# Optimization experiments

Measured on AMD Instinct MI355X. Metric: run time of the kernel, lower is better.

Reference implementation:

```python
import jax, jax.numpy as jnp
import numpy as np

CONV_LAYERS = 1
BI_GRU_LAYERS = 2
BN_EPS = 1e-3


def _bn(x, gamma, beta, mean, var):
    return gamma * (x - mean) * jax.lax.rsqrt(var + BN_EPS) + beta


def _gru_pass(x, Wx, Wh, b_in, b_rec, reverse=False):
    # Keras GRU: reset_after=True, recurrent_activation=sigmoid, activation=relu,
    # gate order [z, r, h]. x: [B,T,D] -> [B,T,U]
    B, T, _ = x.shape
    U = Wh.shape[0]
    if reverse:
        x = x[:, ::-1]
    xg = jnp.einsum('btd,dg->btg', x, Wx) + b_in  # [B,T,3U] input-side gates, precomputed
    xg = jnp.swapaxes(xg, 0, 1)                    # time-major [T,B,3U]

    def step(h, g):
        rg = h @ Wh + b_rec                        # recurrent-side gates [B,3U]
        xz, xr, xh = jnp.split(g, 3, axis=-1)
        rz, rr, rh = jnp.split(rg, 3, axis=-1)
        z = jax.nn.sigmoid(xz + rz)
        r = jax.nn.sigmoid(xr + rr)
        hh = jax.nn.relu(xh + r * rh)              # reset_after: r gates the recurrent term
        h = z * h + (1.0 - z) * hh
        return h, h

    h0 = jnp.zeros((B, U), x.dtype)
    _, hs = jax.lax.scan(step, h0, xg)             # [T,B,U]
    hs = jnp.swapaxes(hs, 0, 1)
    if reverse:
        hs = hs[:, ::-1]
    return hs


def setup_inputs() -> dict:
    key = jax.random.key(0)
    ks = jax.random.split(key, 16)
    B, T, F = 32, 1024, 80
    C, U, V, K = 512, 512, 1024, 11
    s = 0.02
    inp = {
        'x': jax.random.normal(ks[0], (B, T, F), jnp.float32),
        'conv_w': jax.random.normal(ks[1], (K, F, C), jnp.float32) * s,
        'conv_b': jnp.zeros((C,), jnp.float32),
        'gru_fwd_wx': jax.random.normal(ks[2], (C, 3 * U), jnp.float32) * s,
        'gru_fwd_wh': jax.random.normal(ks[3], (U, 3 * U), jnp.float32) * s,
        'gru_fwd_bi': jnp.zeros((3 * U,), jnp.float32),
        'gru_fwd_br': jnp.zeros((3 * U,), jnp.float32),
        'gru_bwd_wx': jax.random.normal(ks[4], (C, 3 * U), jnp.float32) * s,
        'gru_bwd_wh': jax.random.normal(ks[5], (U, 3 * U), jnp.float32) * s,
        'gru_bwd_bi': jnp.zeros((3 * U,), jnp.float32),
        'gru_bwd_br': jnp.zeros((3 * U,), jnp.float32),
        'gamma': jnp.ones((C,), jnp.float32) + 0.1 * jax.random.normal(ks[6], (C,), jnp.float32),
        'beta': 0.1 * jax.random.normal(ks[7], (C,), jnp.float32),
        'mov_mean': jnp.zeros((C,), jnp.float32),
        'mov_var': jnp.ones((C,), jnp.float32),
        'dense_w': jax.random.normal(ks[8], (U, V), jnp.float32) * s,
        'dense_b': jnp.zeros((V,), jnp.float32),
    }
    return inp


def reference(x, conv_w, conv_b, gru_fwd_wx, gru_fwd_wh, gru_fwd_bi, gru_fwd_br,
              gru_bwd_wx, gru_bwd_wh, gru_bwd_bi, gru_bwd_br,
              gamma, beta, mov_mean, mov_var, dense_w, dense_b):
    for _ in range(CONV_LAYERS):
        x = jax.lax.conv_general_dilated(
            x, conv_w, window_strides=(2,), padding='SAME',
            dimension_numbers=('NWC', 'WIO', 'NWC'))
        x = jax.nn.relu(x + conv_b)
    x = _bn(x, gamma, beta, mov_mean, mov_var)  # same BN layer reused in source
    for _ in range(BI_GRU_LAYERS):              # same BiGRU layer (shared weights) reused
        x = (_gru_pass(x, gru_fwd_wx, gru_fwd_wh, gru_fwd_bi, gru_fwd_br, reverse=False)
             + _gru_pass(x, gru_bwd_wx, gru_bwd_wh, gru_bwd_bi, gru_bwd_br, reverse=True))
    x = _bn(x, gamma, beta, mov_mean, mov_var)
    logits = jnp.einsum('btu,uv->btv', x, dense_w) + dense_b
    return jax.nn.softmax(logits, axis=-1)
```

## Files before the change

kernel.cpp:

```cpp
#include <hip/hip_runtime.h>
#include <hip/hip_fp16.h>

#define BB 32
#define CC 512
#define UU 512
#define GG 1536
#define VV 1024
#define TT 512
#define MM (BB*TT)
#define TIN 1024
#define FIN 80
#define EPS 1e-3f
#define SENT 0xFFFFFFFFu

typedef _Float16 h8 __attribute__((ext_vector_type(8)));
typedef float f4 __attribute__((ext_vector_type(4)));

__global__ __launch_bounds__(256) void conv_bn_k(
    const float* __restrict__ x, const float* __restrict__ w, const float* __restrict__ cb,
    const float* __restrict__ gam, const float* __restrict__ bet,
    const float* __restrict__ mu_, const float* __restrict__ var_,
    __half* __restrict__ out)
{
  __shared__ float xs[41*80];
  int tg = blockIdx.x, b = blockIdx.y, ch = blockIdx.z;
  int t0 = tg*16;
  int in0 = t0*2 - 4;
  for (int i = threadIdx.x; i < 41*80; i += 256) {
    int r = i / 80, f = i - r*80;
    int ri = in0 + r;
    xs[i] = (ri >= 0 && ri < TIN) ? x[((size_t)b*TIN + ri)*FIN + f] : 0.f;
  }
  __syncthreads();
  int c = ch*256 + threadIdx.x;
  float acc[16];
  float bv = cb[c];
#pragma unroll
  for (int i = 0; i < 16; i++) acc[i] = bv;
  for (int k = 0; k < 11; k++) {
    for (int f = 0; f < 80; f++) {
      float wv = w[((size_t)k*80 + f)*CC + c];
#pragma unroll
      for (int i = 0; i < 16; i++) acc[i] += xs[(2*i + k)*80 + f] * wv;
    }
  }
  float ga = gam[c], be = bet[c], mu = mu_[c], iv = rsqrtf(var_[c] + EPS);
#pragma unroll
  for (int i = 0; i < 16; i++) {
    float v = fmaxf(acc[i], 0.f);
    out[((size_t)b*TT + t0 + i)*CC + c] = __float2half(ga*(v - mu)*iv + be);
  }
}

__global__ __launch_bounds__(256) void prep_wx_k(
    const float* __restrict__ wxf, const float* __restrict__ wxb,
    __half* __restrict__ of, __half* __restrict__ ob)
{
  __shared__ float tile[64][65];
  int kt = blockIdx.x*64, nt = blockIdx.y*64;
  const float* src = blockIdx.z ? wxb : wxf;
  __half* dst = blockIdx.z ? ob : of;
  for (int i = threadIdx.x; i < 4096; i += 256) {
    int r = i >> 6, c = i & 63;
    tile[r][c] = src[(size_t)(kt+r)*GG + nt + c];
  }
  __syncthreads();
  for (int i = threadIdx.x; i < 4096; i += 256) {
    int r = i >> 6, c = i & 63;
    __half h = __float2half(tile[c][r]);
    dst[(size_t)(nt+r)*1024 + kt + c] = h;
    dst[(size_t)(nt+r)*1024 + 512 + kt + c] = h;
  }
}

__global__ __launch_bounds__(256) void prep_dense_k(
    const float* __restrict__ dw, const float* __restrict__ gam, const float* __restrict__ var_,
    __half* __restrict__ dst)
{
  __shared__ float tile[64][65];
  __shared__ float s64[64];
  int kt = blockIdx.x*64, nt = blockIdx.y*64;
  if (threadIdx.x < 64) {
    int k = kt + threadIdx.x;
    s64[threadIdx.x] = gam[k] * rsqrtf(var_[k] + EPS);
  }
  for (int i = threadIdx.x; i < 4096; i += 256) {
    int r = i >> 6, c = i & 63;
    tile[r][c] = dw[(size_t)(kt+r)*VV + nt + c];
  }
  __syncthreads();
  for (int i = threadIdx.x; i < 4096; i += 256) {
    int r = i >> 6, c = i & 63;
    __half h = __float2half(tile[c][r] * s64[c]);
    dst[(size_t)(nt+r)*1024 + kt + c] = h;
    dst[(size_t)(nt+r)*1024 + 512 + kt + c] = h;
  }
}

__global__ __launch_bounds__(256) void prep_bias_k(
    const float* __restrict__ dw, const float* __restrict__ db,
    const float* __restrict__ gam, const float* __restrict__ bet,
    const float* __restrict__ mu_, const float* __restrict__ var_,
    float* __restrict__ bias2)
{
  int n = blockIdx.x*256 + threadIdx.x;
  float acc = db[n];
  for (int k = 0; k < CC; k++) {
    float o = bet[k] - gam[k]*mu_[k]*rsqrtf(var_[k] + EPS);
    acc += o * dw[(size_t)k*VV + n];
  }
  bias2[n] = acc;
}

template<int OUTH>
__global__ __launch_bounds__(256,2) void hgemm_k(
    const __half* __restrict__ A, const __half* __restrict__ BT,
    const float* __restrict__ bias, void* __restrict__ Cout,
    int M, int N, int K, int lda, int ldb)
{
  __shared__ _Float16 As[128*40];
  __shared__ _Float16 Bs[128*40];
  int m0 = blockIdx.y*128, n0 = blockIdx.x*128;
  int tid = threadIdx.x;
  int l = tid & 63, w = tid >> 6;
  int wr = w >> 1, wc = w & 1;
  int srow = tid >> 1, soff = (tid & 1)*16;
  const __half* ap = A  + (size_t)(m0 + srow)*lda + soff;
  const __half* bp = BT + (size_t)(n0 + srow)*ldb + soff;
  f4 acc[4][4];
#pragma unroll
  for (int i=0;i<4;i++)
#pragma unroll
    for (int j=0;j<4;j++) acc[i][j] = (f4){0.f,0.f,0.f,0.f};

  uint4 av  = *(const uint4*)(ap);
  uint4 av2 = *(const uint4*)(ap + 8);
  uint4 bv  = *(const uint4*)(bp);
  uint4 bv2 = *(const uint4*)(bp + 8);
  int lr = (l & 15), lk = (l >> 4)*8;
  for (int k0 = 0; k0 < K; k0 += 32) {
    __syncthreads();
    *(uint4*)&As[srow*40 + soff]     = av;
    *(uint4*)&As[srow*40 + soff + 8] = av2;
    *(uint4*)&Bs[srow*40 + soff]     = bv;
    *(uint4*)&Bs[srow*40 + soff + 8] = bv2;
    __syncthreads();
    if (k0 + 32 < K) {
      av  = *(const uint4*)(ap + k0 + 32);
      av2 = *(const uint4*)(ap + k0 + 40);
      bv  = *(const uint4*)(bp + k0 + 32);
      bv2 = *(const uint4*)(bp + k0 + 40);
    }
    h8 af[4], bf[4];
#pragma unroll
    for (int i = 0; i < 4; i++)
      af[i] = *(const h8*)&As[(wr*64 + i*16 + lr)*40 + lk];
#pragma unroll
    for (int j = 0; j < 4; j++)
      bf[j] = *(const h8*)&Bs[(wc*64 + j*16 + lr)*40 + lk];
#pragma unroll
    for (int i = 0; i < 4; i++)
#pragma unroll
      for (int j = 0; j < 4; j++)
        acc[i][j] = __builtin_amdgcn_mfma_f32_16x16x32_f16(af[i], bf[j], acc[i][j], 0, 0, 0);
  }
  int cb = n0 + wc*64 + lr;
  int rb = m0 + wr*64 + (l >> 4)*4;
#pragma unroll
  for (int j = 0; j < 4; j++) {
    float bs = bias[cb + j*16];
#pragma unroll
    for (int i = 0; i < 4; i++) {
#pragma unroll
      for (int q = 0; q < 4; q++) {
        float v = acc[i][j][q] + bs;
        int row = rb + i*16 + q, col = cb + j*16;
        if (OUTH) ((__half*)Cout)[(size_t)row*N + col] = __float2half(v);
        else      ((float*)Cout)[(size_t)row*N + col] = v;
      }
    }
  }
}

__global__ __launch_bounds__(256,1) void gru_layer_k(
    const __half* __restrict__ xgf, const __half* __restrict__ xgb,
    const float* __restrict__ whf, const float* __restrict__ whb,
    const float* __restrict__ brf, const float* __restrict__ brb,
    __half* __restrict__ H,
    unsigned* __restrict__ hbL)
{
  int wg  = blockIdx.x & 31;
  int bg  = (blockIdx.x >> 5) & 3;
  int dir = blockIdx.x >> 7;
  int grp = dir*4 + bg;
  const __half* xg = dir ? xgb : xgf;
  const float* wh  = dir ? whb : whf;
  const float* brc = dir ? brb : brf;
  unsigned* hbg = hbL + (size_t)grp*8192;
  int tid = threadIdx.x;
  int u0 = wg*16, b0 = bg*8;
  int l = tid & 63, wv = tid >> 6;

  __shared__ _Float16 hsl[16*512];
  __shared__ float S[4*3*64*4];

  h8 wb[3][4];
  {
    int n = l & 15, kb = (l >> 4)*8;
#pragma unroll
    for (int t = 0; t < 3; t++) {
      int col = t*512 + u0 + n;
#pragma unroll
      for (int ks = 0; ks < 4; ks++) {
        int k0 = wv*128 + ks*32 + kb;
        h8 v;
#pragma unroll
        for (int j = 0; j < 8; j++)
          v[j] = (_Float16)wh[(size_t)(k0+j)*GG + col];
        wb[t][ks] = v;
      }
    }
  }
  for (int i = tid; i < 4096; i += 256)
    *(unsigned*)&hsl[8*512 + i*2] = 0u;

  int gb_ = tid >> 3, up = tid & 7;
  float br3[3][2];
  float hreg[2] = {0.f, 0.f};
  unsigned xzr = 0, xrr = 0, xhr = 0;
  if (tid < 64) {
    int u = u0 + up*2;
#pragma unroll
    for (int g = 0; g < 3; g++) { br3[g][0] = brc[g*512+u]; br3[g][1] = brc[g*512+u+1]; }
    __hip_atomic_store(&hbg[(0*32 + wg)*64 + tid], 0u,
                       __ATOMIC_RELAXED, __HIP_MEMORY_SCOPE_AGENT);
    int t0_ = dir ? 511 : 0;
    const unsigned* xp = (const unsigned*)xg + (size_t)((b0+gb_)*TT + t0_)*768;
    xzr = xp[(u0>>1) + up];
    xrr = xp[256 + (u0>>1) + up];
    xhr = xp[512 + (u0>>1) + up];
  }

  int sidx = tid - 64, srw = sidx >> 2, sq = sidx & 3;

#define STAGE_PHASE(PH) {                                                   \
    const unsigned* gp = &hbg[((PH)*32 + srw)*64 + sq*16];                  \
    uint4 d0, d1, d2, d3;                                                   \
    long guard = 0;                                                         \
    for (;;) {                                                              \
      asm volatile(                                                         \
        "global_load_dwordx4 %0, %4, off sc0 sc1\n\t"                       \
        "global_load_dwordx4 %1, %4, off offset:16 sc0 sc1\n\t"             \
        "global_load_dwordx4 %2, %4, off offset:32 sc0 sc1\n\t"             \
        "global_load_dwordx4 %3, %4, off offset:48 sc0 sc1\n\t"             \
        "s_waitcnt vmcnt(0)"                                                \
        : "=&v"(d0),"=&v"(d1),"=&v"(d2),"=&v"(d3) : "v"(gp) : "memory");    \
      bool ok = (d0.x!=SENT)&(d0.y!=SENT)&(d0.z!=SENT)&(d0.w!=SENT)         \
              & (d1.x!=SENT)&(d1.y!=SENT)&(d1.z!=SENT)&(d1.w!=SENT)         \
              & (d2.x!=SENT)&(d2.y!=SENT)&(d2.z!=SENT)&(d2.w!=SENT)         \
              & (d3.x!=SENT)&(d3.y!=SENT)&(d3.z!=SENT)&(d3.w!=SENT);        \
      if (ok || ++guard > 3000000L) break;                                  \
    }                                                                       \
    int r0_ = sq*2, r1_ = sq*2 + 1, g0_ = srw*2;                            \
    *(uint4*)&hsl[r0_*512 + (((g0_  ) ^ r0_) << 3)] = d0;                   \
    *(uint4*)&hsl[r0_*512 + (((g0_+1) ^ r0_) << 3)] = d1;                   \
    *(uint4*)&hsl[r1_*512 + (((g0_  ) ^ r1_) << 3)] = d2;                   \
    *(uint4*)&hsl[r1_*512 + (((g0_+1) ^ r1_) << 3)] = d3;                   \
  }

  if (tid >= 64 && tid < 192) STAGE_PHASE(0);
  __syncthreads();

  for (int s = 0; s < 512; s++) {
    f4 a0 = (f4){0.f,0.f,0.f,0.f}, a1 = a0, a2 = a0;
#pragma unroll
    for (int ks = 0; ks < 4; ks++) {
      int g = wv*16 + ks*4 + (l >> 4);
      h8 af = *(const h8*)&hsl[(l & 15)*512 + ((g ^ (l & 7)) << 3)];
      a0 = __builtin_amdgcn_mfma_f32_16x16x32_f16(af, wb[0][ks], a0, 0, 0, 0);
      a1 = __builtin_amdgcn_mfma_f32_16x16x32_f16(af, wb[1][ks], a1, 0, 0, 0);
      a2 = __builtin_amdgcn_mfma_f32_16x16x32_f16(af, wb[2][ks], a2, 0, 0, 0);
    }
    *(f4*)&S[((wv*3 + 0)*64 + l)*4] = a0;
    *(f4*)&S[((wv*3 + 1)*64 + l)*4] = a1;
    *(f4*)&S[((wv*3 + 2)*64 + l)*4] = a2;
    if (tid < 64)
      __hip_atomic_store(&hbg[(((s+2)&3)*32 + wg)*64 + tid], SENT,
                         __ATOMIC_RELAXED, __HIP_MEMORY_SCOPE_AGENT);
    __syncthreads();
    int pn = (s + 1) & 3;
    if (tid < 64) {
      int lane_ = (gb_ >> 2)*16 + up*2;
      int q = gb_ & 3;
      float rgv[3][2];
#pragma unroll
      for (int g3 = 0; g3 < 3; g3++) {
#pragma unroll
        for (int e = 0; e < 2; e++) {
          float a = br3[g3][e];
#pragma unroll
          for (int w = 0; w < 4; w++)
            a += S[((w*3 + g3)*64 + lane_ + e)*4 + q];
          rgv[g3][e] = a;
        }
      }
      __half2 xzh = *(__half2*)&xzr, xrh = *(__half2*)&xrr, xhh = *(__half2*)&xhr;
      float2 xzv = __half22float2(xzh), xrv = __half22float2(xrh), xhv = __half22float2(xhh);
      float xzf[2] = {xzv.x, xzv.y}, xrf[2] = {xrv.x, xrv.y}, xhf[2] = {xhv.x, xhv.y};
#pragma unroll
      for (int e = 0; e < 2; e++) {
        float z = 1.f/(1.f + __expf(-(xzf[e] + rgv[0][e])));
        float r = 1.f/(1.f + __expf(-(xrf[e] + rgv[1][e])));
        float hh = fmaxf(xhf[e] + r*rgv[2][e], 0.f);
        hreg[e] = z*hreg[e] + (1.f - z)*hh;
      }
      __half2 hp2 = __floats2half2_rn(hreg[0], hreg[1]);
      unsigned pk = *(unsigned*)&hp2;
      __hip_atomic_store(&hbg[(pn*32 + wg)*64 + tid], pk,
                         __ATOMIC_RELAXED, __HIP_MEMORY_SCOPE_AGENT);
      int t = dir ? (511 - s) : s;
      ((unsigned*)H)[(size_t)((b0+gb_)*TT + t)*512 + dir*256 + (u0>>1) + up] = pk;
      int tn = (dir ? (510 - s) : (s + 1)) & 511;
      const unsigned* xp = (const unsigned*)xg + (size_t)((b0+gb_)*TT + tn)*768;
      xzr = xp[(u0>>1) + up];
      xrr = xp[256 + (u0>>1) + up];
      xhr = xp[512 + (u0>>1) + up];
    } else if (tid < 192) {
      STAGE_PHASE(pn);
    }
    __syncthreads();
  }
#undef STAGE_PHASE
}

__global__ __launch_bounds__(256) void softmax_k(float* __restrict__ p) {
  size_t row = blockIdx.x;
  float* pr = p + row*VV;
  int tid = threadIdx.x;
  float4 v = ((float4*)pr)[tid];
  float m = fmaxf(fmaxf(v.x, v.y), fmaxf(v.z, v.w));
#pragma unroll
  for (int o = 32; o >= 1; o >>= 1) m = fmaxf(m, __shfl_xor(m, o));
  __shared__ float red[4];
  __shared__ float red2[4];
  int w = tid >> 6;
  if ((tid & 63) == 0) red[w] = m;
  __syncthreads();
  m = fmaxf(fmaxf(red[0], red[1]), fmaxf(red[2], red[3]));
  v.x = __expf(v.x - m); v.y = __expf(v.y - m);
  v.z = __expf(v.z - m); v.w = __expf(v.w - m);
  float s = v.x + v.y + v.z + v.w;
#pragma unroll
  for (int o = 32; o >= 1; o >>= 1) s += __shfl_xor(s, o);
  if ((tid & 63) == 0) red2[w] = s;
  __syncthreads();
  s = red2[0] + red2[1] + red2[2] + red2[3];
  float inv = 1.f / s;
  v.x *= inv; v.y *= inv; v.z *= inv; v.w *= inv;
  ((float4*)pr)[tid] = v;
}

extern "C" void kernel_launch(void* const* d_in, const int* in_sizes, int n_in,
                              void* d_out, int out_size, void* d_ws, size_t ws_size,
                              hipStream_t stream) {
  const float* x      = (const float*)d_in[0];
  const float* conv_w = (const float*)d_in[1];
  const float* conv_b = (const float*)d_in[2];
  const float* wx_f   = (const float*)d_in[3];
  const float* wh_f   = (const float*)d_in[4];
  const float* bi_f   = (const float*)d_in[5];
  const float* br_f   = (const float*)d_in[6];
  const float* wx_b   = (const float*)d_in[7];
  const float* wh_b   = (const float*)d_in[8];
  const float* bi_b   = (const float*)d_in[9];
  const float* br_b   = (const float*)d_in[10];
  const float* gam    = (const float*)d_in[11];
  const float* bet    = (const float*)d_in[12];
  const float* mu_    = (const float*)d_in[13];
  const float* var_   = (const float*)d_in[14];
  const float* dw     = (const float*)d_in[15];
  const float* db     = (const float*)d_in[16];

  char* ws = (char*)d_ws;
  __half* xgf   = (__half*)(ws + 0);
  __half* xgb   = (__half*)(ws + 50331648LL);
  __half* WxfT2 = (__half*)(ws + 100663296LL);
  __half* WxbT2 = (__half*)(ws + 103809024LL);
  __half* DwT2  = (__half*)(ws + 106954752LL);
  float*  bias2 = (float*)(ws + 109051904LL);
  __half* c0    = (__half*)(ws + 109056000LL);
  __half* H     = (__half*)(ws + 109056000LL);
  unsigned* hb1 = (unsigned*)(ws + 142610432LL);
  unsigned* hb2 = (unsigned*)(ws + 142872576LL);
  if (ws_size < 143134720ULL) return;
  float* logits = (float*)d_out;

  hipMemsetAsync(hb1, 0xFF, 524288, stream);

  prep_wx_k<<<dim3(8,24,2), 256, 0, stream>>>(wx_f, wx_b, WxfT2, WxbT2);
  prep_dense_k<<<dim3(8,16), 256, 0, stream>>>(dw, gam, var_, DwT2);
  prep_bias_k<<<4, 256, 0, stream>>>(dw, db, gam, bet, mu_, var_, bias2);

  conv_bn_k<<<dim3(32,32,2), 256, 0, stream>>>(x, conv_w, conv_b, gam, bet, mu_, var_, c0);

  hgemm_k<1><<<dim3(12,128), 256, 0, stream>>>(c0, WxfT2, bi_f, xgf, MM, GG, 512, 512, 1024);
  hgemm_k<1><<<dim3(12,128), 256, 0, stream>>>(c0, WxbT2, bi_b, xgb, MM, GG, 512, 512, 1024);
  gru_layer_k<<<256, 256, 0, stream>>>(xgf, xgb, wh_f, wh_b, br_f, br_b, H, hb1);
  hgemm_k<1><<<dim3(12,128), 256, 0, stream>>>(H, WxfT2, bi_f, xgf, MM, GG, 1024, 1024, 1024);
  hgemm_k<1><<<dim3(12,128), 256, 0, stream>>>(H, WxbT2, bi_b, xgb, MM, GG, 1024, 1024, 1024);
  gru_layer_k<<<256, 256, 0, stream>>>(xgf, xgb, wh_f, wh_b, br_f, br_b, H, hb2);
  hgemm_k<0><<<dim3(8,128), 256, 0, stream>>>(H, DwT2, bias2, logits, MM, VV, 1024, 1024, 1024);
  softmax_k<<<MM, 256, 0, stream>>>(logits);
}
```

Baseline: 2.890 ms.

## Repartition GRU recurrence to 64 blocks with full-K per wave and double-buffered h

The persistent GRU kernel now runs 64 blocks instead of 256. Each wave owns 16 hidden units over the full K=512 reduction, using swapped MFMA operands with a 3x16 register-resident weight tile. This removes the cross-wave shared-memory reduction and the separate gate-computing threads, so all lanes do gate math and all threads poll the global h exchange. The h staging in LDS is double-buffered, leaving one barrier per step. The cost is far more registers per thread, more MFMA work per block, and fewer CUs working on the latency-bound recurrence.

```diff
diff --git a/kernel.cpp b/kernel.cpp
--- a/kernel.cpp
+++ b/kernel.cpp
@@ -189,148 +189,138 @@
     __half* __restrict__ H,
     unsigned* __restrict__ hbL)
 {
-  int wg  = blockIdx.x & 31;
-  int bg  = (blockIdx.x >> 5) & 3;
-  int dir = blockIdx.x >> 7;
+  int wg  = blockIdx.x & 7;
+  int bg  = (blockIdx.x >> 3) & 3;
+  int dir = blockIdx.x >> 5;
   int grp = dir*4 + bg;
   const __half* xg = dir ? xgb : xgf;
   const float* wh  = dir ? whb : whf;
   const float* brc = dir ? brb : brf;
   unsigned* hbg = hbL + (size_t)grp*8192;
   int tid = threadIdx.x;
-  int u0 = wg*16, b0 = bg*8;
-  int l = tid & 63, wv = tid >> 6;
-
-  __shared__ _Float16 hsl[16*512];
-  __shared__ float S[4*3*64*4];
-
-  h8 wb[3][4];
+  int L = tid & 63, wv = tid >> 6;
+  int u0 = wg*64, b0 = bg*8;
+
+  __shared__ _Float16 hsl[2][8][512];
+
+  int urow = L & 15, kb = L >> 4;
+  int ubase = u0 + wv*16;
+  h8 wb[3][16];
+#pragma unroll
+  for (int g3 = 0; g3 < 3; g3++)
+#pragma unroll
+    for (int ks = 0; ks < 16; ks++) {
+      h8 v;
+#pragma unroll
+      for (int j = 0; j < 8; j++)
+        v[j] = (_Float16)wh[(size_t)(ks*32 + kb*8 + j)*GG + g3*512 + ubase + urow];
+      wb[g3][ks] = v;
+    }
+
+  int b = L & 15, b7 = L & 7;
+  int myu = ubase + kb*4;
+  float br3[3][4];
+#pragma unroll
+  for (int g3 = 0; g3 < 3; g3++)
+#pragma unroll
+    for (int q = 0; q < 4; q++)
+      br3[g3][q] = brc[g3*512 + myu + q];
+  float hreg[4] = {0.f, 0.f, 0.f, 0.f};
+  bool bval = b < 8;
+  int upair = (u0 >> 1) + wv*8 + kb*2;
+
+  uint2 xz2, xr2, xh2;
   {
-    int n = l & 15, kb = (l >> 4)*8;
-#pragma unroll
-    for (int t = 0; t < 3; t++) {
-      int col = t*512 + u0 + n;
-#pragma unroll
-      for (int ks = 0; ks < 4; ks++) {
-        int k0 = wv*128 + ks*32 + kb;
-        h8 v;
-#pragma unroll
-        for (int j = 0; j < 8; j++)
-          v[j] = (_Float16)wh[(size_t)(k0+j)*GG + col];
-        wb[t][ks] = v;
-      }
-    }
-  }
-  for (int i = tid; i < 4096; i += 256)
-    *(unsigned*)&hsl[8*512 + i*2] = 0u;
-
-  int gb_ = tid >> 3, up = tid & 7;
-  float br3[3][2];
-  float hreg[2] = {0.f, 0.f};
-  unsigned xzr = 0, xrr = 0, xhr = 0;
-  if (tid < 64) {
-    int u = u0 + up*2;
-#pragma unroll
-    for (int g = 0; g < 3; g++) { br3[g][0] = brc[g*512+u]; br3[g][1] = brc[g*512+u+1]; }
-    __hip_atomic_store(&hbg[(0*32 + wg)*64 + tid], 0u,
-                       __ATOMIC_RELAXED, __HIP_MEMORY_SCOPE_AGENT);
     int t0_ = dir ? 511 : 0;
-    const unsigned* xp = (const unsigned*)xg + (size_t)((b0+gb_)*TT + t0_)*768;
-    xzr = xp[(u0>>1) + up];
-    xrr = xp[256 + (u0>>1) + up];
-    xhr = xp[512 + (u0>>1) + up];
-  }
-
-  int sidx = tid - 64, srw = sidx >> 2, sq = sidx & 3;
-
-#define STAGE_PHASE(PH) {                                                   \
-    const unsigned* gp = &hbg[((PH)*32 + srw)*64 + sq*16];                  \
-    uint4 d0, d1, d2, d3;                                                   \
+    const unsigned* xp = (const unsigned*)xg + (size_t)((b0 + b7)*TT + t0_)*768;
+    xz2 = *(const uint2*)(xp + upair);
+    xr2 = *(const uint2*)(xp + 256 + upair);
+    xh2 = *(const uint2*)(xp + 512 + upair);
+  }
+
+  __hip_atomic_store(&hbg[0*2048 + wg*256 + tid], 0u,
+                     __ATOMIC_RELAXED, __HIP_MEMORY_SCOPE_AGENT);
+
+  int sr = tid >> 5, sc = tid & 31;
+  int sb = sc >> 2, sg0 = sr*8 + (sc & 3)*2;
+  int sws0 = ((sg0 ^ sb) << 3), sws1 = (((sg0 + 1) ^ sb) << 3);
+
+#define STAGE(PH, NB) {                                                     \
+    const unsigned* gp = &hbg[(PH)*2048 + sr*256 + sc*8];                   \
+    uint4 d0, d1;                                                           \
     long guard = 0;                                                         \
     for (;;) {                                                              \
       asm volatile(                                                         \
-        "global_load_dwordx4 %0, %4, off sc0 sc1\n\t"                       \
-        "global_load_dwordx4 %1, %4, off offset:16 sc0 sc1\n\t"             \
-        "global_load_dwordx4 %2, %4, off offset:32 sc0 sc1\n\t"             \
-        "global_load_dwordx4 %3, %4, off offset:48 sc0 sc1\n\t"             \
+        "global_load_dwordx4 %0, %2, off sc0 sc1\n\t"                       \
+        "global_load_dwordx4 %1, %2, off offset:16 sc0 sc1\n\t"             \
         "s_waitcnt vmcnt(0)"                                                \
-        : "=&v"(d0),"=&v"(d1),"=&v"(d2),"=&v"(d3) : "v"(gp) : "memory");    \
+        : "=&v"(d0), "=&v"(d1) : "v"(gp) : "memory");                       \
       bool ok = (d0.x!=SENT)&(d0.y!=SENT)&(d0.z!=SENT)&(d0.w!=SENT)         \
-              & (d1.x!=SENT)&(d1.y!=SENT)&(d1.z!=SENT)&(d1.w!=SENT)         \
-              & (d2.x!=SENT)&(d2.y!=SENT)&(d2.z!=SENT)&(d2.w!=SENT)         \
-              & (d3.x!=SENT)&(d3.y!=SENT)&(d3.z!=SENT)&(d3.w!=SENT);        \
+              & (d1.x!=SENT)&(d1.y!=SENT)&(d1.z!=SENT)&(d1.w!=SENT);        \
       if (ok || ++guard > 3000000L) break;                                  \
     }                                                                       \
-    int r0_ = sq*2, r1_ = sq*2 + 1, g0_ = srw*2;                            \
-    *(uint4*)&hsl[r0_*512 + (((g0_  ) ^ r0_) << 3)] = d0;                   \
-    *(uint4*)&hsl[r0_*512 + (((g0_+1) ^ r0_) << 3)] = d1;                   \
-    *(uint4*)&hsl[r1_*512 + (((g0_  ) ^ r1_) << 3)] = d2;                   \
-    *(uint4*)&hsl[r1_*512 + (((g0_+1) ^ r1_) << 3)] = d3;                   \
-  }
-
-  if (tid >= 64 && tid < 192) STAGE_PHASE(0);
+    *(uint4*)&hsl[NB][sb][sws0] = d0;                                       \
+    *(uint4*)&hsl[NB][sb][sws1] = d1;                                       \
+  }
+
+  STAGE(0, 0);
   __syncthreads();
 
   for (int s = 0; s < 512; s++) {
+    int buf = s & 1;
+    __hip_atomic_store(&hbg[((s+3)&3)*2048 + wg*256 + tid], SENT,
+                       __ATOMIC_RELAXED, __HIP_MEMORY_SCOPE_AGENT);
     f4 a0 = (f4){0.f,0.f,0.f,0.f}, a1 = a0, a2 = a0;
 #pragma unroll
-    for (int ks = 0; ks < 4; ks++) {
-      int g = wv*16 + ks*4 + (l >> 4);
-      h8 af = *(const h8*)&hsl[(l & 15)*512 + ((g ^ (l & 7)) << 3)];
-      a0 = __builtin_amdgcn_mfma_f32_16x16x32_f16(af, wb[0][ks], a0, 0, 0, 0);
-      a1 = __builtin_amdgcn_mfma_f32_16x16x32_f16(af, wb[1][ks], a1, 0, 0, 0);
-      a2 = __builtin_amdgcn_mfma_f32_16x16x32_f16(af, wb[2][ks], a2, 0, 0, 0);
-    }
-    *(f4*)&S[((wv*3 + 0)*64 + l)*4] = a0;
-    *(f4*)&S[((wv*3 + 1)*64 + l)*4] = a1;
-    *(f4*)&S[((wv*3 + 2)*64 + l)*4] = a2;
-    if (tid < 64)
-      __hip_atomic_store(&hbg[(((s+2)&3)*32 + wg)*64 + tid], SENT,
-                         __ATOMIC_RELAXED, __HIP_MEMORY_SCOPE_AGENT);
+    for (int ks = 0; ks < 16; ks++) {
+      int g = ks*4 + kb;
+      h8 hf = *(const h8*)&hsl[buf][b7][(g ^ b7) << 3];
+      a0 = __builtin_amdgcn_mfma_f32_16x16x32_f16(wb[0][ks], hf, a0, 0, 0, 0);
+      a1 = __builtin_amdgcn_mfma_f32_16x16x32_f16(wb[1][ks], hf, a1, 0, 0, 0);
+      a2 = __builtin_amdgcn_mfma_f32_16x16x32_f16(wb[2][ks], hf, a2, 0, 0, 0);
+    }
+    int t = dir ? (511 - s) : s;
+    __half2 xzl = *(__half2*)&xz2.x, xzh = *(__half2*)&xz2.y;
+    __half2 xrl = *(__half2*)&xr2.x, xrh = *(__half2*)&xr2.y;
+    __half2 xhl = *(__half2*)&xh2.x, xhh = *(__half2*)&xh2.y;
+    float2 fz0 = __half22float2(xzl), fz1 = __half22float2(xzh);
+    float2 fr0 = __half22float2(xrl), fr1 = __half22float2(xrh);
+    float2 fh0 = __half22float2(xhl), fh1 = __half22float2(xhh);
+    float xzf[4] = {fz0.x, fz0.y, fz1.x, fz1.y};
+    float xrf[4] = {fr0.x, fr0.y, fr1.x, fr1.y};
+    float xhf[4] = {fh0.x, fh0.y, fh1.x, fh1.y};
+#pragma unroll
+    for (int q = 0; q < 4; q++) {
+      float az = (q==0? a0[0] : q==1? a0[1] : q==2? a0[2] : a0[3]);
+      float ar = (q==0? a1[0] : q==1? a1[1] : q==2? a1[2] : a1[3]);
+      float ah = (q==0? a2[0] : q==1? a2[1] : q==2? a2[2] : a2[3]);
+      float z = 1.f/(1.f + __expf(-(xzf[q] + br3[0][q] + az)));
+      float r = 1.f/(1.f + __expf(-(xrf[q] + br3[1][q] + ar)));
+      float hh = fmaxf(xhf[q] + r*(br3[2][q] + ah), 0.f);
+      hreg[q] = z*hreg[q] + (1.f - z)*hh;
+    }
+    int pn = (s + 1) & 3;
+    if (bval) {
+      __half2 p01 = __floats2half2_rn(hreg[0], hreg[1]);
+      __half2 p23 = __floats2half2_rn(hreg[2], hreg[3]);
+      unsigned pk0 = *(unsigned*)&p01, pk1 = *(unsigned*)&p23;
+      unsigned long pkl = ((unsigned long)pk1 << 32) | pk0;
+      __hip_atomic_store((unsigned long*)&hbg[pn*2048 + wg*256 + b*32 + wv*8 + kb*2],
+                         pkl, __ATOMIC_RELAXED, __HIP_MEMORY_SCOPE_AGENT);
+      uint2 pv; pv.x = pk0; pv.y = pk1;
+      *(uint2*)((unsigned*)H + (size_t)((b0 + b)*TT + t)*512 + dir*256 + upair) = pv;
+    }
+    {
+      int tn = (dir ? (510 - s) : (s + 1)) & 511;
+      const unsigned* xp = (const unsigned*)xg + (size_t)((b0 + b7)*TT + tn)*768;
+      xz2 = *(const uint2*)(xp + upair);
+      xr2 = *(const uint2*)(xp + 256 + upair);
+      xh2 = *(const uint2*)(xp + 512 + upair);
+    }
+    if (s < 511) STAGE(pn, buf ^ 1);
     __syncthreads();
-    int pn = (s + 1) & 3;
-    if (tid < 64) {
-      int lane_ = (gb_ >> 2)*16 + up*2;
-      int q = gb_ & 3;
-      float rgv[3][2];
-#pragma unroll
-      for (int g3 = 0; g3 < 3; g3++) {
-#pragma unroll
-        for (int e = 0; e < 2; e++) {
-          float a = br3[g3][e];
-#pragma unroll
-          for (int w = 0; w < 4; w++)
-            a += S[((w*3 + g3)*64 + lane_ + e)*4 + q];
-          rgv[g3][e] = a;
-        }
-      }
-      __half2 xzh = *(__half2*)&xzr, xrh = *(__half2*)&xrr, xhh = *(__half2*)&xhr;
-      float2 xzv = __half22float2(xzh), xrv = __half22float2(xrh), xhv = __half22float2(xhh);
-      float xzf[2] = {xzv.x, xzv.y}, xrf[2] = {xrv.x, xrv.y}, xhf[2] = {xhv.x, xhv.y};
-#pragma unroll
-      for (int e = 0; e < 2; e++) {
-        float z = 1.f/(1.f + __expf(-(xzf[e] + rgv[0][e])));
-        float r = 1.f/(1.f + __expf(-(xrf[e] + rgv[1][e])));
-        float hh = fmaxf(xhf[e] + r*rgv[2][e], 0.f);
-        hreg[e] = z*hreg[e] + (1.f - z)*hh;
-      }
-      __half2 hp2 = __floats2half2_rn(hreg[0], hreg[1]);
-      unsigned pk = *(unsigned*)&hp2;
-      __hip_atomic_store(&hbg[(pn*32 + wg)*64 + tid], pk,
-                         __ATOMIC_RELAXED, __HIP_MEMORY_SCOPE_AGENT);
-      int t = dir ? (511 - s) : s;
-      ((unsigned*)H)[(size_t)((b0+gb_)*TT + t)*512 + dir*256 + (u0>>1) + up] = pk;
-      int tn = (dir ? (510 - s) : (s + 1)) & 511;
-      const unsigned* xp = (const unsigned*)xg + (size_t)((b0+gb_)*TT + tn)*768;
-      xzr = xp[(u0>>1) + up];
-      xrr = xp[256 + (u0>>1) + up];
-      xhr = xp[512 + (u0>>1) + up];
-    } else if (tid < 192) {
-      STAGE_PHASE(pn);
-    }
-    __syncthreads();
-  }
-#undef STAGE_PHASE
+  }
+#undef STAGE
 }
 
 __global__ __launch_bounds__(256) void softmax_k(float* __restrict__ p) {
@@ -405,10 +395,10 @@
 
   hgemm_k<1><<<dim3(12,128), 256, 0, stream>>>(c0, WxfT2, bi_f, xgf, MM, GG, 512, 512, 1024);
   hgemm_k<1><<<dim3(12,128), 256, 0, stream>>>(c0, WxbT2, bi_b, xgb, MM, GG, 512, 512, 1024);
-  gru_layer_k<<<256, 256, 0, stream>>>(xgf, xgb, wh_f, wh_b, br_f, br_b, H, hb1);
+  gru_layer_k<<<64, 256, 0, stream>>>(xgf, xgb, wh_f, wh_b, br_f, br_b, H, hb1);
   hgemm_k<1><<<dim3(12,128), 256, 0, stream>>>(H, WxfT2, bi_f, xgf, MM, GG, 1024, 1024, 1024);
   hgemm_k<1><<<dim3(12,128), 256, 0, stream>>>(H, WxbT2, bi_b, xgb, MM, GG, 1024, 1024, 1024);
-  gru_layer_k<<<256, 256, 0, stream>>>(xgf, xgb, wh_f, wh_b, br_f, br_b, H, hb2);
+  gru_layer_k<<<64, 256, 0, stream>>>(xgf, xgb, wh_f, wh_b, br_f, br_b, H, hb2);
   hgemm_k<0><<<dim3(8,128), 256, 0, stream>>>(H, DwT2, bias2, logits, MM, VV, 1024, 1024, 1024);
   softmax_k<<<MM, 256, 0, stream>>>(logits);
 }
```

New measurement: 2.830 ms. 1.02x faster.
